# Optimization experiments

Hardware: AMD Instinct MI355X
Metric: run time of the kernel (lower is better)

Reference implementation:

```python
import jax, jax.numpy as jnp
import numpy as np

B, D, K = 4096, 2048, 16384
SIDE = int(np.sqrt(K))  # 128


def setup_inputs() -> dict:
    key = jax.random.key(0)
    k1, k2 = jax.random.split(key)
    x = jax.random.normal(k1, (B, D), dtype=jnp.float32)
    # GlorotNormal for shape (D, K): std = sqrt(2/(D+K))
    glorot_std = np.sqrt(2.0 / (D + K)).astype(np.float32)
    kernel = jax.random.normal(k2, (D, K), dtype=jnp.float32) * glorot_std
    sigma = jnp.asarray(2.0, dtype=jnp.float32)  # STM sigma weight (non-trainable)
    return {"x": x, "kernel": kernel, "sigma": sigma}


def _stm_forward(x, kernel, sigma):
    # norms2[b,k] = || x[b,:] - kernel[:,k] ||^2, computed via the Gram expansion
    # (same math as the broadcast-subtract-norm, without the [B,D,K] intermediate).
    x2 = jnp.sum(x * x, axis=1, keepdims=True)            # [B,1]
    k2 = jnp.sum(kernel * kernel, axis=0, keepdims=True)  # [1,K]
    norms2 = jnp.maximum(x2 - 2.0 * (x @ kernel) + k2, 0.0)  # [B,K]

    # winner-take-all: argmin over prototypes -> 2D grid coordinate
    idx = jnp.argmin(norms2, axis=1)                      # [B] int
    wx = (idx // SIDE).astype(jnp.float32)                # [B]
    wy = (idx % SIDE).astype(jnp.float32)                 # [B]

    # grid point p has coords (p // SIDE, p % SIDE) per make_grid()
    p = jnp.arange(K)
    gx = (p // SIDE).astype(jnp.float32)                  # [K]
    gy = (p % SIDE).astype(jnp.float32)                   # [K]

    d2 = (gx[None, :] - wx[:, None]) ** 2 + (gy[None, :] - wy[:, None]) ** 2  # [B,K]
    radials = jnp.exp(-0.5 * d2 / (sigma * sigma))
    radials = radials / (sigma * np.sqrt(2.0 * np.pi).astype(np.float32))
    return radials * norms2                               # [B,K]


def reference(x, kernel, sigma):
    return _stm_forward(x, kernel, sigma)
```

## Files before the change

kernel.cpp:

```cpp
#include <hip/hip_runtime.h>
#include <math.h>

#define B_    4096
#define D_    2048
#define K_    16384
#define SIDE  128

#define BM 128
#define BN 128
#define BD 16
#define ASTR 132

#define EPS_CAND 0.04f
#define MARGIN   0.015f
#define MAXCAND  64
#define RMAX     12

#define NKT 64

typedef __attribute__((ext_vector_type(8))) short bf16x8;
typedef __attribute__((ext_vector_type(4))) float f32x4;

__device__ __forceinline__ short bf16_rne(float f) {
    unsigned u = __float_as_uint(f);
    unsigned r = u + 0x7FFFu + ((u >> 16) & 1u);
    return (short)(r >> 16);
}

__device__ __forceinline__ void gload16(const void* g, void* l) {
    __builtin_amdgcn_global_load_lds(
        (const __attribute__((address_space(1))) unsigned int*)g,
        (__attribute__((address_space(3))) unsigned int*)l, 16, 0, 0);
}

__global__ __launch_bounds__(256) void pack_a_x2(const float* __restrict__ x,
                                                 short* __restrict__ Ah,
                                                 float* __restrict__ x2) {
    const int row = blockIdx.x;
    const int t = threadIdx.x;
    const size_t i = (size_t)row * 2048 + (size_t)t * 8;
    float4 v0 = *(const float4*)&x[i];
    float4 v1 = *(const float4*)&x[i + 4];
    short tmp[8] = { bf16_rne(v0.x), bf16_rne(v0.y), bf16_rne(v0.z), bf16_rne(v0.w),
                     bf16_rne(v1.x), bf16_rne(v1.y), bf16_rne(v1.z), bf16_rne(v1.w) };
    *(int4*)&Ah[i] = *(const int4*)tmp;
    float s = v0.x*v0.x + v0.y*v0.y + v0.z*v0.z + v0.w*v0.w
            + v1.x*v1.x + v1.y*v1.y + v1.z*v1.z + v1.w*v1.w;
    __shared__ float red[256];
    red[t] = s; __syncthreads();
    for (int off = 128; off > 0; off >>= 1) {
        if (t < off) red[t] += red[t + off];
        __syncthreads();
    }
    if (t == 0) x2[row] = red[0];
}

__global__ __launch_bounds__(256) void pack_bt_k2(const float* __restrict__ kmat,
                                                  short* __restrict__ Bt,
                                                  float* __restrict__ pk2b) {
    __shared__ float tile[64][65];
    const int n0 = blockIdx.x * 64, d0 = blockIdx.y * 64;
    const int t = threadIdx.x;
    const int lr = t >> 4, lc4 = (t & 15) * 4;
    #pragma unroll
    for (int r = 0; r < 4; ++r) {
        float4 v = *(const float4*)&kmat[(size_t)(d0 + lr + r*16) * K_ + n0 + lc4];
        tile[lr + r*16][lc4 + 0] = v.x;
        tile[lr + r*16][lc4 + 1] = v.y;
        tile[lr + r*16][lc4 + 2] = v.z;
        tile[lr + r*16][lc4 + 3] = v.w;
    }
    __syncthreads();
    const int n = t >> 2, dc = (t & 3) * 16;
    short tmp[16];
    float s = 0.f;
    #pragma unroll
    for (int i = 0; i < 16; ++i) {
        float v = tile[dc + i][n];
        tmp[i] = bf16_rne(v);
        s = fmaf(v, v, s);
    }
    short* dst = &Bt[(size_t)(n0 + n) * 2048 + d0 + dc];
    *(int4*)dst       = *(const int4*)tmp;
    *(int4*)(dst + 8) = *(const int4*)(tmp + 8);
    s += __shfl_xor(s, 1);
    s += __shfl_xor(s, 2);
    if ((t & 3) == 0) pk2b[(size_t)(d0 >> 6) * K_ + n0 + n] = s;
}

__global__ void k2_reduce32(const float* __restrict__ pk2b, float* __restrict__ k2) {
    int k = blockIdx.x * 256 + threadIdx.x;
    float s = 0.f;
    #pragma unroll
    for (int j = 0; j < 32; ++j) s += pk2b[(size_t)j * K_ + k];
    k2[k] = s;
}

__global__ __launch_bounds__(512, 2) void gemm_8ph(
    const short* __restrict__ Ah, const short* __restrict__ Bt,
    const float* __restrict__ x2, const float* __restrict__ k2,
    float* __restrict__ out, float* __restrict__ pmin)
{
    __shared__ short As[4 * 8192];
    __shared__ short Bs[4 * 8192];

    const int tid = threadIdx.x;
    const int lane = tid & 63;
    const int w = tid >> 6;
    const int wm = w >> 2, wn = w & 3;
    const int lrow = lane & 15, lkg = lane >> 4;

    const int orig = blockIdx.x;
    const int xcd = orig & 7, seq = orig >> 3;
    const int bn0 = (xcd * 8 + (seq & 7)) * 256;
    const int bm0 = (seq >> 3) * 256;

    const int csw = ((tid & 3) ^ ((tid >> 3) & 3)) * 8;
    const short* pA = Ah + (size_t)(bm0 + (tid >> 2)) * 2048 + csw;
    const short* pB = Bt + (size_t)(bn0 + (tid >> 2)) * 2048 + csw;
    const int ldsT = tid * 8;

    const int rsw = (lkg ^ ((lrow >> 1) & 3)) * 8;
    const int aBase = (wm * 128 + lrow) * 32 + rsw;
    const int bBase = (wn * 64 + lrow) * 32 + rsw;

    f32x4 acc[8][4];
    #pragma unroll
    for (int i = 0; i < 8; ++i)
        #pragma unroll
        for (int j = 0; j < 4; ++j) acc[i][j] = (f32x4){0.f, 0.f, 0.f, 0.f};

#define STAGE(T) do { \
    short* _la = As + (((T) & 3) * 8192) + ldsT; \
    const short* _ga = pA + (size_t)(T) * 32; \
    gload16(_ga, _la); \
    gload16(_ga + (size_t)128 * 2048, _la + 4096); \
    short* _lb = Bs + (((T) & 3) * 8192) + ldsT; \
    const short* _gb = pB + (size_t)(T) * 32; \
    gload16(_gb, _lb); \
    gload16(_gb + (size_t)128 * 2048, _lb + 4096); \
} while (0)

#define READ12(AR, BR, REG) do { \
    const short* _a = &As[(REG) * 8192]; \
    const short* _b = &Bs[(REG) * 8192]; \
    _Pragma("unroll") \
    for (int nf = 0; nf < 4; ++nf) (BR)[nf] = *(const bf16x8*)&_b[bBase + nf * 512]; \
    _Pragma("unroll") \
    for (int mf = 0; mf < 8; ++mf) (AR)[mf] = *(const bf16x8*)&_a[aBase + mf * 512]; \
} while (0)

#define MFMA32(AR, BR) do { \
    __builtin_amdgcn_s_setprio(1); \
    _Pragma("unroll") \
    for (int mf = 0; mf < 8; ++mf) { \
        acc[mf][0] = __builtin_amdgcn_mfma_f32_16x16x32_bf16((AR)[mf], (BR)[0], acc[mf][0], 0, 0, 0); \
        acc[mf][1] = __builtin_amdgcn_mfma_f32_16x16x32_bf16((AR)[mf], (BR)[1], acc[mf][1], 0, 0, 0); \
        acc[mf][2] = __builtin_amdgcn_mfma_f32_16x16x32_bf16((AR)[mf], (BR)[2], acc[mf][2], 0, 0, 0); \
        acc[mf][3] = __builtin_amdgcn_mfma_f32_16x16x32_bf16((AR)[mf], (BR)[3], acc[mf][3], 0, 0, 0); \
    } \
    __builtin_amdgcn_s_setprio(0); \
} while (0)

#define TILE_END(T) do { \
    if ((T) < NKT - 3) asm volatile("s_waitcnt vmcnt(4)" ::: "memory"); \
    else               asm volatile("s_waitcnt vmcnt(0)" ::: "memory"); \
    __builtin_amdgcn_s_barrier(); \
    asm volatile("" ::: "memory"); \
} while (0)

    bf16x8 aA[8], bA[4], aB[8], bB[4];

    STAGE(0); STAGE(1); STAGE(2);
    asm volatile("s_waitcnt vmcnt(4)" ::: "memory");
    __builtin_amdgcn_s_barrier();
    asm volatile("" ::: "memory");
    READ12(aA, bA, 0);

    for (int t = 0; t < NKT; t += 2) {
        if (t + 3 < NKT) STAGE(t + 3);
        READ12(aB, bB, (t + 1) & 3);
        __builtin_amdgcn_sched_barrier(0);
        MFMA32(aA, bA);
        TILE_END(t);

        if (t + 4 < NKT) STAGE(t + 4);
        if (t + 2 < NKT) READ12(aA, bA, (t + 2) & 3);
        __builtin_amdgcn_sched_barrier(0);
        MFMA32(aB, bB);
        TILE_END(t + 1);
    }
#undef STAGE
#undef READ12
#undef MFMA32
#undef TILE_END

    const int r0 = bm0 + wm * 128 + lkg * 4;
    const int c0 = bn0 + wn * 64 + lrow;
    float kc[4];
    #pragma unroll
    for (int nf = 0; nf < 4; ++nf) kc[nf] = k2[c0 + nf * 16];

    float* sm2 = (float*)As;
    __syncthreads();

    #pragma unroll
    for (int mf = 0; mf < 8; ++mf) {
        #pragma unroll
        for (int jj = 0; jj < 4; ++jj) {
            const int gr = r0 + mf * 16 + jj;
            const float xv = x2[gr];
            float* orow = out + (size_t)gr * K_ + c0;
            float v0 = fmaxf((xv - 2.f * acc[mf][0][jj]) + kc[0], 0.f);
            float v1 = fmaxf((xv - 2.f * acc[mf][1][jj]) + kc[1], 0.f);
            float v2 = fmaxf((xv - 2.f * acc[mf][2][jj]) + kc[2], 0.f);
            float v3 = fmaxf((xv - 2.f * acc[mf][3][jj]) + kc[3], 0.f);
            orow[0]  = v0;
            orow[16] = v1;
            orow[32] = v2;
            orow[48] = v3;
            float m = fminf(fminf(v0, v1), fminf(v2, v3));
            m = fminf(m, __shfl_xor(m, 1));
            m = fminf(m, __shfl_xor(m, 2));
            m = fminf(m, __shfl_xor(m, 4));
            m = fminf(m, __shfl_xor(m, 8));
            if (lrow == 0)
                sm2[wn * 256 + wm * 128 + mf * 16 + lkg * 4 + jj] = m;
        }
    }
    __syncthreads();
    if (tid < 256) {
        float m = fminf(fminf(sm2[tid], sm2[256 + tid]),
                        fminf(sm2[512 + tid], sm2[768 + tid]));
        pmin[(size_t)(bn0 >> 8) * 4096 + bm0 + tid] = m;
    }
}

__global__ __launch_bounds__(256) void rowpost(
    float* __restrict__ out, const float* __restrict__ X,
    const float* __restrict__ Kmat, const float* __restrict__ pmin,
    const float* __restrict__ sigma)
{
    const int row = blockIdx.x;
    const int t = threadIdx.x;
    float* orow = out + (size_t)row * K_;

    __shared__ float sblk[64];
    __shared__ float sgmin;
    __shared__ int scnt, swidx, needRefine;
    __shared__ int cand[MAXCAND];
    __shared__ float cval[MAXCAND];
    __shared__ double sred[256];
    __shared__ float cscore[MAXCAND];
    __shared__ float patch[(2*RMAX+1)*(2*RMAX+1)];

    if (t < 64) sblk[t] = pmin[(size_t)t * 4096 + row];
    if (t == 0) scnt = 0;
    __syncthreads();
    if (t == 0) {
        float m = sblk[0];
        for (int i = 1; i < 64; ++i) m = fminf(m, sblk[i]);
        sgmin = m;
    }
    __syncthreads();
    const float thr = sgmin + EPS_CAND;

    for (int b = 0; b < 64; ++b) {
        if (sblk[b] <= thr) {
            float v = orow[b * 256 + t];
            if (v <= thr) {
                int p = atomicAdd(&scnt, 1);
                if (p < MAXCAND) { cand[p] = b * 256 + t; cval[p] = v; }
            }
        }
    }
    __syncthreads();
    const int cnt = min(scnt, MAXCAND);

    if (cnt == 1) {
        if (t == 0) { swidx = cand[0]; needRefine = 0; }
        __syncthreads();
    } else {
        if (t == 0) {
            float bv = cval[0]; int bi = cand[0];
            for (int c = 1; c < cnt; ++c)
                if (cval[c] < bv || (cval[c] == bv && cand[c] < bi)) { bv = cval[c]; bi = cand[c]; }
            float sv = 3.4e38f;
            for (int c = 0; c < cnt; ++c)
                if (cand[c] != bi) sv = fminf(sv, cval[c]);
            if (sv - bv > MARGIN) { swidx = bi; needRefine = 0; }
            else needRefine = 1;
        }
        __syncthreads();
        if (needRefine) {
            const float* xrow = X + (size_t)row * D_;
            double xs = 0.0;
            for (int d = t; d < D_; d += 256) {
                float xv = xrow[d];
                float sq = xv * xv;
                xs += (double)sq;
            }
            sred[t] = xs; __syncthreads();
            for (int off = 128; off > 0; off >>= 1) {
                if (t < off) sred[t] += sred[t + off];
                __syncthreads();
            }
            const float x2f = (float)sred[0];
            __syncthreads();

            for (int c = 0; c < cnt; ++c) {
                const int k = cand[c];
                double dt = 0.0, kk = 0.0;
                for (int d = t; d < D_; d += 256) {
                    float wv = Kmat[(size_t)d * K_ + k];
                    float xv = xrow[d];
                    dt += (double)xv * (double)wv;
                    float w2 = wv * wv;
                    kk += (double)w2;
                }
                sred[t] = dt; __syncthreads();
                for (int off = 128; off > 0; off >>= 1) {
                    if (t < off) sred[t] += sred[t + off];
                    __syncthreads();
                }
                const float dotf = (float)sred[0];
                __syncthreads();
                sred[t] = kk; __syncthreads();
                for (int off = 128; off > 0; off >>= 1) {
                    if (t < off) sred[t] += sred[t + off];
                    __syncthreads();
                }
                if (t == 0) {
                    const float k2f = (float)sred[0];
                    cscore[c] = fmaxf((x2f - 2.0f * dotf) + k2f, 0.0f);
                }
                __syncthreads();
            }
            if (t == 0) {
                float bv = cscore[0]; int bi = cand[0];
                for (int c = 1; c < cnt; ++c) {
                    if (cscore[c] < bv || (cscore[c] == bv && cand[c] < bi)) {
                        bv = cscore[c]; bi = cand[c];
                    }
                }
                swidx = bi;
            }
            __syncthreads();
        }
    }

    const int wi = swidx;
    const int wx = wi >> 7, wy = wi & 127;
    const float sg = sigma[0];
    const float ninv  = -0.5f / (sg * sg);
    const float scale = 1.0f / (sg * sqrtf(2.0f * 3.14159265358979323846f));
    float larg = 8192.0f * scale;
    int R = (larg <= 1.0f) ? 0
          : (int)ceilf(sg * sqrtf(2.0f * logf(larg)));

    if (R <= RMAX) {
        const int W = 2 * R + 1;
        for (int p = t; p < W * W; p += 256) {
            int dx = p / W - R, dy = p % W - R;
            int gx = wx + dx, gy = wy + dy;
            if ((unsigned)gx < 128u && (unsigned)gy < 128u)
                patch[p] = orow[gx * 128 + gy];
        }
        __syncthreads();
        for (int i = t; i < K_ / 4; i += 256) {
            const int k0 = i * 4;
            const int gx = k0 >> 7;
            const int dx = gx - wx;
            float4 v = make_float4(0.f, 0.f, 0.f, 0.f);
            float* vp = (float*)&v;
            if (dx >= -R && dx <= R) {
                #pragma unroll
                for (int j = 0; j < 4; ++j) {
                    int gy = (k0 & 127) + j;
                    int dy = gy - wy;
                    if (dy >= -R && dy <= R) {
                        float d2 = (float)(dx * dx + dy * dy);
                        vp[j] = patch[(dx + R) * W + (dy + R)] * (scale * __expf(ninv * d2));
                    }
                }
            }
            *(float4*)&orow[k0] = v;
        }
    } else {
        for (int i = t; i < K_ / 4; i += 256) {
            float4 v = ((const float4*)orow)[i];
            float* vp = (float*)&v;
            #pragma unroll
            for (int j = 0; j < 4; ++j) {
                int k = i * 4 + j;
                float gx = (float)(k >> 7), gy = (float)(k & 127);
                float dx = gx - (float)wx, dy = gy - (float)wy;
                float d2 = dx * dx + dy * dy;
                vp[j] = vp[j] * (__expf(ninv * d2) * scale);
            }
            ((float4*)orow)[i] = v;
        }
    }
}

__global__ void k2_partial(const float* __restrict__ kmat, float* __restrict__ pk2) {
    int k  = blockIdx.x * 256 + threadIdx.x;
    int d0 = blockIdx.y * 256;
    float s = 0.f;
    #pragma unroll 8
    for (int d = 0; d < 256; ++d) {
        float v = kmat[(size_t)(d0 + d) * K_ + k];
        s = fmaf(v, v, s);
    }
    pk2[(size_t)blockIdx.y * K_ + k] = s;
}

__global__ void k2_reduce(const float* __restrict__ pk2, float* __restrict__ k2) {
    int k = blockIdx.x * 256 + threadIdx.x;
    float s = 0.f;
    #pragma unroll
    for (int j = 0; j < 8; ++j) s += pk2[(size_t)j * K_ + k];
    k2[k] = s;
}

__global__ void x2_kernel(const float* __restrict__ x, float* __restrict__ x2) {
    int row = blockIdx.x;
    const float* xr = x + (size_t)row * D_;
    int t = threadIdx.x;
    float4 v0 = ((const float4*)xr)[t];
    float4 v1 = ((const float4*)xr)[t + 256];
    float s = v0.x*v0.x + v0.y*v0.y + v0.z*v0.z + v0.w*v0.w
            + v1.x*v1.x + v1.y*v1.y + v1.z*v1.z + v1.w*v1.w;
    __shared__ float red[256];
    red[t] = s; __syncthreads();
    for (int off = 128; off > 0; off >>= 1) {
        if (t < off) red[t] += red[t + off];
        __syncthreads();
    }
    if (t == 0) x2[row] = red[0];
}

__global__ __launch_bounds__(256) void gemm_norms(
    const float* __restrict__ X, const float* __restrict__ Kmat,
    const float* __restrict__ x2, const float* __restrict__ k2,
    float* __restrict__ out)
{
    __shared__ float Asf[BD * ASTR];
    __shared__ float Bsf[BD * BN];

    const int tid = threadIdx.x;
    const int tx = tid & 15, ty = tid >> 4;
    const int bn0 = blockIdx.x * BN;
    const int bm0 = blockIdx.y * BM;

    float acc[8][8];
    #pragma unroll
    for (int i = 0; i < 8; ++i)
        #pragma unroll
        for (int j = 0; j < 8; ++j) acc[i][j] = 0.f;

    const int lm = tid >> 2;
    const int ld = (tid & 3) << 2;
    const int bd = tid >> 5;
    const int bk = (tid & 31) << 2;

    const float* Xp = X    + (size_t)(bm0 + lm) * D_ + ld;
    const float* Kp = Kmat + (size_t)bd * K_ + bn0 + bk;

    float4 a0 = *(const float4*)(Xp);
    float4 a1 = *(const float4*)(Xp + (size_t)64 * D_);
    float4 b0 = *(const float4*)(Kp);
    float4 b1 = *(const float4*)(Kp + (size_t)8 * K_);

    const int NT = D_ / BD;
    for (int kt = 0; kt < NT; ++kt) {
        __syncthreads();
        Asf[(ld+0)*ASTR + lm]      = a0.x;
        Asf[(ld+1)*ASTR + lm]      = a0.y;
        Asf[(ld+2)*ASTR + lm]      = a0.z;
        Asf[(ld+3)*ASTR + lm]      = a0.w;
        Asf[(ld+0)*ASTR + lm + 64] = a1.x;
        Asf[(ld+1)*ASTR + lm + 64] = a1.y;
        Asf[(ld+2)*ASTR + lm + 64] = a1.z;
        Asf[(ld+3)*ASTR + lm + 64] = a1.w;
        *(float4*)&Bsf[bd*BN + bk]     = b0;
        *(float4*)&Bsf[(bd+8)*BN + bk] = b1;
        __syncthreads();

        if (kt + 1 < NT) {
            const float* Xn = Xp + (kt + 1) * BD;
            const float* Kn = Kp + (size_t)(kt + 1) * BD * K_;
            a0 = *(const float4*)(Xn);
            a1 = *(const float4*)(Xn + (size_t)64 * D_);
            b0 = *(const float4*)(Kn);
            b1 = *(const float4*)(Kn + (size_t)8 * K_);
        }

        #pragma unroll
        for (int dd = 0; dd < BD; ++dd) {
            float4 A0 = *(const float4*)&Asf[dd*ASTR + ty*4];
            float4 A1 = *(const float4*)&Asf[dd*ASTR + ty*4 + 64];
            float4 B0 = *(const float4*)&Bsf[dd*BN + tx*4];
            float4 B1 = *(const float4*)&Bsf[dd*BN + tx*4 + 64];
            float a[8] = {A0.x,A0.y,A0.z,A0.w,A1.x,A1.y,A1.z,A1.w};
            float b[8] = {B0.x,B0.y,B0.z,B0.w,B1.x,B1.y,B1.z,B1.w};
            #pragma unroll
            for (int i = 0; i < 8; ++i)
                #pragma unroll
                for (int j = 0; j < 8; ++j)
                    acc[i][j] = fmaf(a[i], b[j], acc[i][j]);
        }
    }

    int rl[8], cl[8];
    #pragma unroll
    for (int i = 0; i < 4; ++i) {
        rl[i] = ty*4 + i;  rl[i+4] = ty*4 + 64 + i;
        cl[i] = tx*4 + i;  cl[i+4] = tx*4 + 64 + i;
    }
    float xr[8], kc[8];
    #pragma unroll
    for (int i = 0; i < 8; ++i) { xr[i] = x2[bm0 + rl[i]]; kc[i] = k2[bn0 + cl[i]]; }

    #pragma unroll
    for (int i = 0; i < 8; ++i) {
        float vv[8];
        #pragma unroll
        for (int j = 0; j < 8; ++j)
            vv[j] = fmaxf((xr[i] - 2.f * acc[i][j]) + kc[j], 0.f);
        int gr = bm0 + rl[i];
        *(float4*)&out[(size_t)gr * K_ + bn0 + tx*4]      = make_float4(vv[0],vv[1],vv[2],vv[3]);
        *(float4*)&out[(size_t)gr * K_ + bn0 + tx*4 + 64] = make_float4(vv[4],vv[5],vv[6],vv[7]);
    }
}

__global__ __launch_bounds__(256) void rowscan(
    const float* __restrict__ out, const float* __restrict__ X,
    const float* __restrict__ Kmat, int* __restrict__ widx)
{
    const int row = blockIdx.x;
    const int t = threadIdx.x;
    const float* orow = out + (size_t)row * K_;

    float mn = 3.4e38f;
    for (int i = t; i < K_/4; i += 256) {
        float4 v = ((const float4*)orow)[i];
        mn = fminf(mn, fminf(fminf(v.x, v.y), fminf(v.z, v.w)));
    }
    __shared__ float smin[256];
    smin[t] = mn; __syncthreads();
    for (int off = 128; off > 0; off >>= 1) {
        if (t < off) smin[t] = fminf(smin[t], smin[t+off]);
        __syncthreads();
    }
    const float rowmin = smin[0];

    __shared__ int scnt;
    __shared__ int cand[MAXCAND];
    if (t == 0) scnt = 0;
    __syncthreads();
    const float thr = rowmin + EPS_CAND;
    for (int i = t; i < K_/4; i += 256) {
        float4 v = ((const float4*)orow)[i];
        float vv[4] = {v.x, v.y, v.z, v.w};
        #pragma unroll
        for (int j = 0; j < 4; ++j) {
            if (vv[j] <= thr) {
                int p = atomicAdd(&scnt, 1);
                if (p < MAXCAND) cand[p] = i*4 + j;
            }
        }
    }
    __syncthreads();
    const int cnt = min(scnt, MAXCAND);
    if (cnt == 1) {
        if (t == 0) widx[row] = cand[0];
        return;
    }

    const float* xrow = X + (size_t)row * D_;
    __shared__ double sred[256];
    double xs = 0.0;
    for (int d = t; d < D_; d += 256) {
        float xv = xrow[d];
        float sq = xv * xv;
        xs += (double)sq;
    }
    sred[t] = xs; __syncthreads();
    for (int off = 128; off > 0; off >>= 1) {
        if (t < off) sred[t] += sred[t+off];
        __syncthreads();
    }
    const float x2f = (float)sred[0];
    __syncthreads();

    __shared__ float cscore[MAXCAND];
    for (int c = 0; c < cnt; ++c) {
        const int k = cand[c];
        double dt = 0.0, kk = 0.0;
        for (int d = t; d < D_; d += 256) {
            float wv = Kmat[(size_t)d * K_ + k];
            float xv = xrow[d];
            dt += (double)xv * (double)wv;
            float w2 = wv * wv;
            kk += (double)w2;
        }
        sred[t] = dt; __syncthreads();
        for (int off = 128; off > 0; off >>= 1) {
            if (t < off) sred[t] += sred[t+off];
            __syncthreads();
        }
        const float dotf = (float)sred[0];
        __syncthreads();
        sred[t] = kk; __syncthreads();
        for (int off = 128; off > 0; off >>= 1) {
            if (t < off) sred[t] += sred[t+off];
            __syncthreads();
        }
        if (t == 0) {
            const float k2f = (float)sred[0];
            cscore[c] = fmaxf((x2f - 2.0f * dotf) + k2f, 0.0f);
        }
        __syncthreads();
    }
    if (t == 0) {
        float bv = cscore[0]; int bi = cand[0];
        for (int c = 1; c < cnt; ++c) {
            if (cscore[c] < bv || (cscore[c] == bv && cand[c] < bi)) {
                bv = cscore[c]; bi = cand[c];
            }
        }
        widx[row] = bi;
    }
}

__global__ void finalize(float* __restrict__ out, const int* __restrict__ widx,
                         const float* __restrict__ sigma) {
    size_t gid = (size_t)blockIdx.x * blockDim.x + threadIdx.x;
    int row = (int)(gid / (K_ / 4));
    int c4  = (int)(gid % (K_ / 4)) * 4;
    int w = widx[row];
    float wx = (float)(w >> 7), wy = (float)(w & 127);
    float sg = sigma[0];
    float ninv  = -0.5f / (sg * sg);
    float scale = 1.0f / (sg * sqrtf(2.0f * 3.14159265358979323846f));
    float4 v = *(float4*)&out[(size_t)row * K_ + c4];
    float* vp = (float*)&v;
    #pragma unroll
    for (int j = 0; j < 4; ++j) {
        int k = c4 + j;
        float gx = (float)(k >> 7), gy = (float)(k & 127);
        float dx = gx - wx, dy = gy - wy;
        float d2 = dx*dx + dy*dy;
        vp[j] = vp[j] * (__expf(ninv * d2) * scale);
    }
    *(float4*)&out[(size_t)row * K_ + c4] = v;
}

extern "C" void kernel_launch(void* const* d_in, const int* in_sizes, int n_in,
                              void* d_out, int out_size, void* d_ws, size_t ws_size,
                              hipStream_t stream) {
    const float* x     = (const float*)d_in[0];
    const float* kmat  = (const float*)d_in[1];
    const float* sigma = (const float*)d_in[2];
    float* out = (float*)d_out;

    const size_t BT_BYTES = (size_t)K_ * D_ * 2;
    const size_t AH_BYTES = (size_t)B_ * D_ * 2;
    const size_t WS_NEED  = BT_BYTES + AH_BYTES +
        (size_t)(16384 + 4096 + 32*16384 + 64*4096) * 4;

    if (ws_size >= WS_NEED) {
        short* Bt   = (short*)d_ws;
        short* Ahp  = (short*)((char*)d_ws + BT_BYTES);
        float* k2   = (float*)((char*)d_ws + BT_BYTES + AH_BYTES);
        float* x2   = k2 + 16384;
        float* pk2b = x2 + 4096;
        float* pmin = pk2b + 32*16384;

        pack_a_x2 <<<B_, 256, 0, stream>>>(x, Ahp, x2);
        pack_bt_k2<<<dim3(K_/64, D_/64), 256, 0, stream>>>(kmat, Bt, pk2b);
        k2_reduce32<<<K_/256, 256, 0, stream>>>(pk2b, k2);
        gemm_8ph  <<<1024, 512, 0, stream>>>(Ahp, Bt, x2, k2, out, pmin);
        rowpost   <<<B_, 256, 0, stream>>>(out, x, kmat, pmin, sigma);
    } else {
        float* ws = (float*)d_ws;
        float* k2   = ws;
        float* x2   = ws + 16384;
        int*   widx = (int*)(ws + 20480);
        float* pk2  = ws + 24576;

        k2_partial<<<dim3(K_/256, 8), 256, 0, stream>>>(kmat, pk2);
        k2_reduce <<<K_/256, 256, 0, stream>>>(pk2, k2);
        x2_kernel <<<B_, 256, 0, stream>>>(x, x2);
        gemm_norms<<<dim3(K_/BN, B_/BM), 256, 0, stream>>>(x, kmat, x2, k2, out);
        rowscan   <<<B_, 256, 0, stream>>>(out, x, kmat, widx);
        finalize  <<<(size_t)B_ * (K_/4) / 256, 256, 0, stream>>>(out, widx, sigma);
    }
}
```

Baseline: 501.2 us.

## Restructure GEMM main loop to one barrier per two K-tiles

The bf16 MFMA main loop changes from a per-tile wait and barrier to a double-step schedule. Each step stages two future tiles into the 4-slot LDS ring and interleaves the next tile's LDS reads between the two MFMA blocks. It then does a single full vmcnt/lgkmcnt wait and barrier. This halves barrier count, but waiting for all outstanding global loads every step means prefetches have only two tiles of compute to land, which may expose memory latency.

```diff
diff --git a/kernel.cpp b/kernel.cpp
--- a/kernel.cpp
+++ b/kernel.cpp
@@ -162,38 +162,36 @@
     __builtin_amdgcn_s_setprio(0); \
 } while (0)
 
-#define TILE_END(T) do { \
-    if ((T) < NKT - 3) asm volatile("s_waitcnt vmcnt(4)" ::: "memory"); \
-    else               asm volatile("s_waitcnt vmcnt(0)" ::: "memory"); \
-    __builtin_amdgcn_s_barrier(); \
-    asm volatile("" ::: "memory"); \
-} while (0)
-
     bf16x8 aA[8], bA[4], aB[8], bB[4];
 
-    STAGE(0); STAGE(1); STAGE(2);
-    asm volatile("s_waitcnt vmcnt(4)" ::: "memory");
+    STAGE(0); STAGE(1); STAGE(2); STAGE(3);
+    asm volatile("s_waitcnt vmcnt(8)" ::: "memory");
     __builtin_amdgcn_s_barrier();
     asm volatile("" ::: "memory");
     READ12(aA, bA, 0);
-
-    for (int t = 0; t < NKT; t += 2) {
-        if (t + 3 < NKT) STAGE(t + 3);
-        READ12(aB, bB, (t + 1) & 3);
+    READ12(aB, bB, 1);
+    asm volatile("s_waitcnt vmcnt(0) lgkmcnt(0)" ::: "memory");
+    __builtin_amdgcn_s_barrier();
+    asm volatile("" ::: "memory");
+
+    for (int s = 0; s < NKT / 2; ++s) {
+        const int t0 = 2 * s;
+        if (t0 + 4 < NKT) STAGE(t0 + 4);
+        if (t0 + 5 < NKT) STAGE(t0 + 5);
         __builtin_amdgcn_sched_barrier(0);
+
         MFMA32(aA, bA);
-        TILE_END(t);
-
-        if (t + 4 < NKT) STAGE(t + 4);
-        if (t + 2 < NKT) READ12(aA, bA, (t + 2) & 3);
-        __builtin_amdgcn_sched_barrier(0);
+        if (t0 + 2 < NKT) READ12(aA, bA, (t0 + 2) & 3);
         MFMA32(aB, bB);
-        TILE_END(t + 1);
+        if (t0 + 3 < NKT) READ12(aB, bB, (t0 + 3) & 3);
+
+        asm volatile("s_waitcnt vmcnt(0) lgkmcnt(0)" ::: "memory");
+        __builtin_amdgcn_s_barrier();
+        asm volatile("" ::: "memory");
     }
 #undef STAGE
 #undef READ12
 #undef MFMA32
-#undef TILE_END
 
     const int r0 = bm0 + wm * 128 + lkg * 4;
     const int c0 = bn0 + wn * 64 + lrow;
```

New measurement: 467.1 us. 1.07x faster.
